# Kernel optimization log

Hardware: AMD Instinct MI355X
Metric: run time of the kernel (lower is better)

Reference implementation:

```python
import jax, jax.numpy as jnp
import numpy as np
from math import log2, ceil

NUM_LEAVES = 128
KERNEL = 8
STRIDE = 8
PADDING = 0
LR = 0.3

LEAF_NUM = 2 ** ceil(log2(NUM_LEAVES))   # 128
DEPTH = int(log2(LEAF_NUM))              # 7
NUM_NODES = 2 * LEAF_NUM - 1             # 255


def _ancestor_table():
    # A[j-1, t-1] = global heap index of the ancestor of node j at tree level t,
    # or -1 if t exceeds j's own level. Nodes use heap indexing: children of i
    # are 2i+1, 2i+2 (matches the layer bookkeeping in the torch module).
    A = np.full((NUM_NODES - 1, DEPTH), -1, dtype=np.int32)
    for j in range(1, NUM_NODES):
        lvl = int(np.floor(np.log2(j + 1)))
        anc = j
        for t in range(lvl, 0, -1):
            A[j - 1, t - 1] = anc
            anc = (anc - 1) // 2
    return jnp.asarray(A)

_ANC = _ancestor_table()  # (NUM_NODES-1, DEPTH)


def img2patches(x):
    x = jnp.pad(x, PADDING)
    H, W = x.shape
    n0 = (H - KERNEL) // STRIDE + 1
    n1 = (W - KERNEL) // STRIDE + 1
    win = jnp.arange(KERNEL)
    rows = jnp.arange(n0)[:, None] * STRIDE + win[None, :]  # (n0, k)
    cols = jnp.arange(n1)[:, None] * STRIDE + win[None, :]  # (n1, k)
    p = x[rows[:, None, :, None], cols[None, :, None, :]]   # (n0, n1, k, k)
    return p.reshape(n0 * n1, KERNEL * KERNEL)


def setup_inputs() -> dict:
    key = jax.random.key(0)
    k1, k2 = jax.random.split(key)
    image = jax.random.uniform(k1, (2048, 2048), dtype=jnp.float32)
    nodes = jax.random.uniform(k2, (NUM_NODES, KERNEL * KERNEL), dtype=jnp.float32)
    return {"image": image, "nodes": nodes}


def reference(image, nodes):
    X = img2patches(image)                      # (P, k^2)
    P = X.shape[0]

    # --- hierarchical BMU descent (binary tree, DEPTH levels) ---
    cur = jnp.zeros((P,), dtype=jnp.int32)      # root
    bmu_levels = []
    for _ in range(DEPTH):
        c0 = 2 * cur + 1
        c1 = 2 * cur + 2
        # pnorm with p=2 in the source is (sum((a-b)^2))^2 -- monotone, kept faithful
        d0 = jnp.sum((nodes[c0] - X) ** 2, axis=-1) ** 2
        d1 = jnp.sum((nodes[c1] - X) ** 2, axis=-1) ** 2
        cur = jnp.where(d1 < d0, c1, c0)        # tie -> first (c0), like torch.min
        bmu_levels.append(cur)
    bmu_path = jnp.stack(bmu_levels, axis=1)    # (P, DEPTH), bmu at levels 1..DEPTH

    # --- layer_state for every non-root node: number of levels at which the
    # node's ancestor coincides with the BMU chain (== the torch concatenated
    # layer_state, columns ordered by global node index 1..NUM_NODES-1) ---
    state = jnp.sum(_ANC[None, :, :] == bmu_path[:, None, :], axis=-1)  # (P, N-1)

    lrates = LR * (2.0 ** jnp.arange(1, DEPTH + 2, dtype=jnp.float32)) / 2.0 ** (DEPTH + 1)
    lrs = lrates[state]                          # (P, N-1)

    # mean_p lrs[p,j] * (X[p,:] - nodes[1+j,:])
    #   = (lrs^T @ X)/P - mean_p(lrs)[:,None] * nodes[1:]
    upd = jnp.einsum('pj,pk->jk', lrs, X) / P - lrs.mean(axis=0)[:, None] * nodes[1:]
    new_nodes = nodes.at[1:].add(upd)

    return new_nodes, cur[:, None]               # updated codebook, leaf BMU per patch
```

## Files before the change

kernel.cpp:

```cpp
#include <hip/hip_runtime.h>

#define IMG_W 2048
#define NUM_NODES 255
#define NLEAF 128
#define DEPTH 7
#define RS 68

template<int CTRL>
__device__ __forceinline__ float dpp_add(float x) {
    int v = __builtin_amdgcn_update_dpp(0, __float_as_int(x), CTRL, 0xF, 0xF, true);
    return x + __int_as_float(v);
}
__device__ __forceinline__ float group16_sum(float x) {
    x = dpp_add<0xB1>(x);
    x = dpp_add<0x4E>(x);
    x = dpp_add<0x141>(x);
    x = dpp_add<0x128>(x);
    return x;
}

__global__ __launch_bounds__(1024, 4) void fusedK(const float* __restrict__ img,
                                                  const float* __restrict__ nodes,
                                                  float* __restrict__ leaf_out,
                                                  float* __restrict__ S,
                                                  unsigned* __restrict__ cnt)
{
    __shared__ float nds[NUM_NODES * RS];
    __shared__ float Sl[NLEAF * RS];
    __shared__ unsigned cntl[NLEAF];

    const int t = threadIdx.x;
    const int b = blockIdx.x;
    const int g = t >> 4;
    const int q = t & 15;
    const int q4 = q * 4;

    for (int i = t; i < NLEAF * RS; i += 1024) Sl[i] = 0.0f;
    if (t < NLEAF) cntl[t] = 0u;

    const float4* ng = (const float4*)nodes;
    for (int i = t; i < NUM_NODES * 16; i += 1024) {
        *(float4*)&nds[(i >> 4) * RS + (i & 15) * 4] = ng[i];
    }

    float4 xv[4];
    #pragma unroll
    for (int ch = 0; ch < 4; ++ch) {
        const int p = b * 256 + ch * 64 + g;
        const int r = p >> 8, c = p & 255;
        xv[ch] = *(const float4*)(img + (size_t)(r * 8 + (q >> 1)) * IMG_W + c * 8 + (q & 1) * 4);
    }
    __syncthreads();

    #pragma unroll
    for (int ch = 0; ch < 4; ++ch) {
        const float4 x = xv[ch];
        int cur = 0;
        #pragma unroll
        for (int lvl = 0; lvl < DEPTH; ++lvl) {
            const int c0 = 2 * cur + 1;
            const float* base = &nds[c0 * RS + q4];
            const float4 a  = *(const float4*)(base);
            const float4 bb = *(const float4*)(base + RS);
            float s0 = 0.f, s1 = 0.f, d;
            d = a.x  - x.x; s0 = fmaf(d, d, s0);
            d = a.y  - x.y; s0 = fmaf(d, d, s0);
            d = a.z  - x.z; s0 = fmaf(d, d, s0);
            d = a.w  - x.w; s0 = fmaf(d, d, s0);
            d = bb.x - x.x; s1 = fmaf(d, d, s1);
            d = bb.y - x.y; s1 = fmaf(d, d, s1);
            d = bb.z - x.z; s1 = fmaf(d, d, s1);
            d = bb.w - x.w; s1 = fmaf(d, d, s1);
            s0 = group16_sum(s0);
            s1 = group16_sum(s1);
            cur = (s1 < s0) ? (c0 + 1) : c0;
        }

        const int L = cur - 127;
        if (q == 0) {
            leaf_out[b * 256 + ch * 64 + g] = (float)cur;
            atomicAdd(&cntl[L], 1u);
        }
        float* dst = &Sl[L * RS + q4];
        atomicAdd(dst + 0, x.x);
        atomicAdd(dst + 1, x.y);
        atomicAdd(dst + 2, x.z);
        atomicAdd(dst + 3, x.w);
    }
    __syncthreads();

    for (int i = t; i < NLEAF * 64; i += 1024) {
        const float v = Sl[(i >> 6) * RS + (i & 63)];
        if (v != 0.0f) atomicAdd(&S[i], v);
    }
    if (t < NLEAF && cntl[t] != 0u) atomicAdd(&cnt[t], cntl[t]);
}

__global__ __launch_bounds__(256) void updateK(const float* __restrict__ nodes,
                                               const float* __restrict__ S,
                                               const unsigned* __restrict__ cnt,
                                               float* __restrict__ out)
{
    const int gid = blockIdx.x * 256 + threadIdx.x;
    if (gid >= NUM_NODES * 64) return;
    const int n = gid >> 6, k = gid & 63;
    const float nd = nodes[gid];
    if (n == 0) { out[gid] = nd; return; }

    const int pos = n + 1;
    const int Ln = 31 - __clz(pos);
    float su = 0.f, sc = 0.f;
    #pragma unroll 8
    for (int L = 0; L < NLEAF; ++L) {
        const int a = (128 + L) >> (7 - Ln);
        const int x = pos ^ a;
        const int state = (x == 0) ? Ln : (Ln - (31 - __clz(x)) - 1);
        const float lr = 0.3f * ((float)(1 << state) * (1.0f / 128.0f));
        su = fmaf(lr, S[L * 64 + k], su);
        sc = fmaf(lr, (float)cnt[L], sc);
    }
    const float invP = 1.0f / 65536.0f;
    out[gid] = nd + su * invP - (sc * invP) * nd;
}

extern "C" void kernel_launch(void* const* d_in, const int* in_sizes, int n_in,
                              void* d_out, int out_size, void* d_ws, size_t ws_size,
                              hipStream_t stream)
{
    const float* img   = (const float*)d_in[0];
    const float* nodes = (const float*)d_in[1];

    float* out_nodes = (float*)d_out;
    float* out_leaf  = out_nodes + NUM_NODES * 64;

    float*    S   = (float*)d_ws;
    unsigned* cnt = (unsigned*)(S + NLEAF * 64);

    hipMemsetAsync(d_ws, 0, (NLEAF * 64) * sizeof(float) + NLEAF * sizeof(unsigned), stream);
    fusedK<<<256, 1024, 0, stream>>>(img, nodes, out_leaf, S, cnt);
    updateK<<<64, 256, 0, stream>>>(nodes, S, cnt, out_nodes);
}
```

Baseline: 108.8 us.

## Replace global atomics with per-block partial sums and a separate reduce kernel

The fused kernel no longer atomically adds its leaf sums and counts into global memory. Each block now writes dense partials to the workspace, and a new reduceK kernel sums the 256 partials deterministically. The leaf accumulator aliases the node shared buffer, which cuts LDS use and may allow more blocks per CU, at the cost of an extra barrier and a separate accumulation phase. This removes the memset but adds a kernel launch and roughly 8 MB of partial-sum traffic.

Result: slower. 122.9 us (+13.0%).

```diff
diff --git a/kernel.cpp b/kernel.cpp
--- a/kernel.cpp
+++ b/kernel.cpp
@@ -5,6 +5,7 @@
 #define NLEAF 128
 #define DEPTH 7
 #define RS 68
+#define NBLK 256
 
 template<int CTRL>
 __device__ __forceinline__ float dpp_add(float x) {
@@ -22,12 +23,12 @@
 __global__ __launch_bounds__(1024, 4) void fusedK(const float* __restrict__ img,
                                                   const float* __restrict__ nodes,
                                                   float* __restrict__ leaf_out,
-                                                  float* __restrict__ S,
-                                                  unsigned* __restrict__ cnt)
+                                                  float* __restrict__ S_partial,
+                                                  unsigned* __restrict__ cnt_partial)
 {
     __shared__ float nds[NUM_NODES * RS];
-    __shared__ float Sl[NLEAF * RS];
     __shared__ unsigned cntl[NLEAF];
+    float* Sl = nds;
 
     const int t = threadIdx.x;
     const int b = blockIdx.x;
@@ -35,7 +36,6 @@
     const int q = t & 15;
     const int q4 = q * 4;
 
-    for (int i = t; i < NLEAF * RS; i += 1024) Sl[i] = 0.0f;
     if (t < NLEAF) cntl[t] = 0u;
 
     const float4* ng = (const float4*)nodes;
@@ -52,6 +52,7 @@
     }
     __syncthreads();
 
+    int leaf[4];
     #pragma unroll
     for (int ch = 0; ch < 4; ++ch) {
         const float4 x = xv[ch];
@@ -75,25 +76,58 @@
             s1 = group16_sum(s1);
             cur = (s1 < s0) ? (c0 + 1) : c0;
         }
+        leaf[ch] = cur;
+        if (q == 0) leaf_out[b * 256 + ch * 64 + g] = (float)cur;
+    }
+    __syncthreads();
 
-        const int L = cur - 127;
-        if (q == 0) {
-            leaf_out[b * 256 + ch * 64 + g] = (float)cur;
-            atomicAdd(&cntl[L], 1u);
-        }
+    for (int i = t; i < NLEAF * RS; i += 1024) Sl[i] = 0.0f;
+    __syncthreads();
+
+    #pragma unroll
+    for (int ch = 0; ch < 4; ++ch) {
+        const int L = leaf[ch] - 127;
+        const float4 x = xv[ch];
         float* dst = &Sl[L * RS + q4];
         atomicAdd(dst + 0, x.x);
         atomicAdd(dst + 1, x.y);
         atomicAdd(dst + 2, x.z);
         atomicAdd(dst + 3, x.w);
+        if (q == 0) atomicAdd(&cntl[L], 1u);
     }
     __syncthreads();
 
-    for (int i = t; i < NLEAF * 64; i += 1024) {
-        const float v = Sl[(i >> 6) * RS + (i & 63)];
-        if (v != 0.0f) atomicAdd(&S[i], v);
+    float4* Sp = (float4*)(S_partial + (size_t)b * (NLEAF * 64));
+    for (int i = t; i < NLEAF * 16; i += 1024) {
+        const int row = i >> 4, qq = i & 15;
+        Sp[i] = *(const float4*)&Sl[row * RS + qq * 4];
     }
-    if (t < NLEAF && cntl[t] != 0u) atomicAdd(&cnt[t], cntl[t]);
+    if (t < NLEAF) cnt_partial[b * NLEAF + t] = cntl[t];
+}
+
+__global__ __launch_bounds__(256) void reduceK(const float* __restrict__ S_partial,
+                                               const unsigned* __restrict__ cnt_partial,
+                                               float* __restrict__ S,
+                                               unsigned* __restrict__ cnt)
+{
+    const int e = blockIdx.x * 256 + threadIdx.x;
+    float a0 = 0.f, a1 = 0.f, a2 = 0.f, a3 = 0.f, a4 = 0.f, a5 = 0.f, a6 = 0.f, a7 = 0.f;
+    for (int b = 0; b < NBLK; b += 8) {
+        a0 += S_partial[(size_t)(b + 0) * 8192 + e];
+        a1 += S_partial[(size_t)(b + 1) * 8192 + e];
+        a2 += S_partial[(size_t)(b + 2) * 8192 + e];
+        a3 += S_partial[(size_t)(b + 3) * 8192 + e];
+        a4 += S_partial[(size_t)(b + 4) * 8192 + e];
+        a5 += S_partial[(size_t)(b + 5) * 8192 + e];
+        a6 += S_partial[(size_t)(b + 6) * 8192 + e];
+        a7 += S_partial[(size_t)(b + 7) * 8192 + e];
+    }
+    S[e] = ((a0 + a1) + (a2 + a3)) + ((a4 + a5) + (a6 + a7));
+    if (e < NLEAF) {
+        unsigned c = 0;
+        for (int b = 0; b < NBLK; ++b) c += cnt_partial[b * NLEAF + e];
+        cnt[e] = c;
+    }
 }
 
 __global__ __launch_bounds__(256) void updateK(const float* __restrict__ nodes,
@@ -133,10 +167,12 @@
     float* out_nodes = (float*)d_out;
     float* out_leaf  = out_nodes + NUM_NODES * 64;
 
-    float*    S   = (float*)d_ws;
-    unsigned* cnt = (unsigned*)(S + NLEAF * 64);
+    float*    S_partial   = (float*)d_ws;
+    unsigned* cnt_partial = (unsigned*)(S_partial + NBLK * 8192);
+    float*    S           = (float*)(cnt_partial + NBLK * NLEAF);
+    unsigned* cnt         = (unsigned*)(S + 8192);
 
-    hipMemsetAsync(d_ws, 0, (NLEAF * 64) * sizeof(float) + NLEAF * sizeof(unsigned), stream);
-    fusedK<<<256, 1024, 0, stream>>>(img, nodes, out_leaf, S, cnt);
+    fusedK<<<NBLK, 1024, 0, stream>>>(img, nodes, out_leaf, S_partial, cnt_partial);
+    reduceK<<<32, 256, 0, stream>>>(S_partial, cnt_partial, S, cnt);
     updateK<<<64, 256, 0, stream>>>(nodes, S, cnt, out_nodes);
 }
```
